# Kernel optimization log

Measured on AMD Instinct MI355X. Metric: run time of the kernel, lower is better.

The kernel has to match this reference:

```python
import jax, jax.numpy as jnp
import numpy as np

B, S, H = 2, 2048, 2048
NH, NKV, HD = 16, 8, 128        # head_dim = H // NH
WINDOW = 1024                    # sliding window size
THETA = 100000.0                 # rope_theta (RotaryEmbedding base)


def setup_inputs() -> dict:
    key = jax.random.key(0)
    ks = jax.random.split(key, 5)
    hidden = jax.random.normal(ks[0], (B, S, H), jnp.float32)
    # fused QKV projection: [H, NH*HD + 2*NKV*HD]
    W_pack = jax.random.normal(ks[1], (H, NH * HD + 2 * NKV * HD), jnp.float32) * (H ** -0.5)
    W_o = jax.random.normal(ks[2], (NH * HD, H), jnp.float32) * ((NH * HD) ** -0.5)
    # per-KV-head 2-tap causal conv weights, softmax-normalized (as in nn.Parameter init)
    conv_k = jax.nn.softmax(jax.random.normal(ks[3], (NKV, 2), jnp.float32), axis=-1)
    conv_v = jax.nn.softmax(jax.random.normal(ks[4], (NKV, 2), jnp.float32), axis=-1)
    return {"hidden": hidden, "W_pack": W_pack, "W_o": W_o, "conv_k": conv_k, "conv_v": conv_v}


def _rope(x, cos, sin):
    # x: (b, s, h, d); cos/sin: (s, d//2); non-interleaved (rotate-half) form
    d2 = x.shape[-1] // 2
    x1, x2 = x[..., :d2], x[..., d2:]
    c = cos[None, :, None, :]
    s = sin[None, :, None, :]
    return jnp.concatenate([x1 * c - x2 * s, x2 * c + x1 * s], axis=-1)


def _causal_conv2(x, w):
    # x: (b, s, kv, d); w: (kv, 2). out[t] = w0*x[t-1] + w1*x[t], zero-padded at t=0
    x_prev = jnp.pad(x, ((0, 0), (1, 0), (0, 0), (0, 0)))[:, :-1]
    return w[None, None, :, 0:1] * x_prev + w[None, None, :, 1:2] * x


def reference(hidden, W_pack, W_o, conv_k, conv_v):
    b, s, _ = hidden.shape
    qkv = hidden @ W_pack                                  # (b, s, NH*HD + 2*NKV*HD)
    q = qkv[..., : NH * HD].reshape(b, s, NH, HD)
    k = qkv[..., NH * HD : NH * HD + NKV * HD].reshape(b, s, NKV, HD)
    v = qkv[..., NH * HD + NKV * HD :].reshape(b, s, NKV, HD)

    inv_freq = 1.0 / (THETA ** (jnp.arange(0, HD, 2, dtype=jnp.float32) / HD))
    freqs = jnp.outer(jnp.arange(s, dtype=jnp.float32), inv_freq)  # (s, HD/2)
    cos, sin = jnp.cos(freqs), jnp.sin(freqs)
    q = _rope(q, cos, sin)
    k = _rope(k, cos, sin)

    # learned 2-tap causal conv mixing adjacent K/V states, per KV head
    k = _causal_conv2(k, conv_k)
    v = _causal_conv2(v, conv_v)

    # GQA: repeat kv heads to match query heads
    group = NH // NKV
    k = jnp.repeat(k, group, axis=2)  # (b, s, NH, HD)
    v = jnp.repeat(v, group, axis=2)

    scores = jnp.einsum('bqhd,bkhd->bhqk', q, k) / jnp.sqrt(jnp.float32(HD))
    i = jnp.arange(s)[:, None]
    j = jnp.arange(s)[None, :]
    mask = (j <= i) & (i - j < WINDOW)  # causal sliding-window mask
    scores = jnp.where(mask[None, None], scores, jnp.finfo(scores.dtype).min)
    probs = jax.nn.softmax(scores, axis=-1)
    out = jnp.einsum('bhqk,bkhd->bqhd', probs, v).reshape(b, s, NH * HD)
    return out @ W_o
```

## Files before the change

kernel.cpp:

```cpp
#include <hip/hip_runtime.h>

#define DI __device__ __forceinline__

typedef unsigned short u16;
typedef __attribute__((ext_vector_type(8))) short s16x8;
typedef __attribute__((ext_vector_type(8))) unsigned short u16x8;
typedef __attribute__((ext_vector_type(4))) float f32x4;
typedef __attribute__((ext_vector_type(16))) float f32x16;

DI u16 f2bf(float x) {
  union { float f; unsigned u; } a; a.f = x;
  unsigned r = a.u + 0x7FFFu + ((a.u >> 16) & 1u);
  return (u16)(r >> 16);
}
DI float bf2f(u16 u) {
  union { unsigned u; float f; } a; a.u = ((unsigned)u) << 16;
  return a.f;
}
DI void gload16(const void* g, void* l) {
  __builtin_amdgcn_global_load_lds(
      (const __attribute__((address_space(1))) unsigned int*)g,
      (__attribute__((address_space(3))) unsigned int*)l, 16, 0, 0);
}
DI f32x4 mfma16(s16x8 a, s16x8 b, f32x4 c) {
  return __builtin_amdgcn_mfma_f32_16x16x32_bf16(a, b, c, 0, 0, 0);
}
DI f32x16 mfma32(s16x8 a, s16x8 b, f32x16 c) {
  return __builtin_amdgcn_mfma_f32_32x32x16_bf16(a, b, c, 0, 0, 0);
}

DI void store_out(float* p, float v) { *p = v; }
DI void store_out(u16* p, float v) { *p = f2bf(v); }

#define SBAR() asm volatile("s_barrier" ::: "memory")
#define WAIT_LGKM0() do { asm volatile("s_waitcnt lgkmcnt(0)" ::: "memory"); \
                          __builtin_amdgcn_sched_barrier(0); } while (0)

__global__ void cvt_kernel(const float* __restrict__ in, u16* __restrict__ out, int n8) {
  int i = blockIdx.x * 256 + threadIdx.x;
  if (i >= n8) return;
  const float4* p = (const float4*)in + (size_t)i * 2;
  float4 a = p[0], b = p[1];
  u16x8 o;
  o[0] = f2bf(a.x); o[1] = f2bf(a.y); o[2] = f2bf(a.z); o[3] = f2bf(a.w);
  o[4] = f2bf(b.x); o[5] = f2bf(b.y); o[6] = f2bf(b.z); o[7] = f2bf(b.w);
  *((u16x8*)out + i) = o;
}

__global__ void cvt_t_kernel(const float* __restrict__ W, u16* __restrict__ Wt, int R, int C) {
  __shared__ u16 tile[64][65];
  int c0 = blockIdx.x * 64, r0 = blockIdx.y * 64;
  int t = threadIdx.x;
#pragma unroll
  for (int i = 0; i < 16; ++i) {
    int flat = i * 256 + t;
    int r = flat >> 6, c = flat & 63;
    tile[r][c] = f2bf(W[(size_t)(r0 + r) * C + (c0 + c)]);
  }
  __syncthreads();
#pragma unroll
  for (int i = 0; i < 16; ++i) {
    int flat = i * 256 + t;
    int c = flat >> 6, r = flat & 63;
    Wt[(size_t)(c0 + c) * R + (r0 + r)] = tile[r][c];
  }
}

__global__ void rope_table_kernel(float* __restrict__ cosT, float* __restrict__ sinT) {
  int i = blockIdx.x * 256 + threadIdx.x;
  int s = i >> 6, d = i & 63;
  float inv = expf(-(float)d * (11.5129254649702295f / 64.f));
  float f = (float)s * inv;
  cosT[i] = cosf(f);
  sinT[i] = sinf(f);
}

template <typename OutT>
__global__ __launch_bounds__(512, 2) void gemm8p_kernel(
    const u16* __restrict__ A, const u16* __restrict__ Bt, OutT* __restrict__ C,
    int M, int N, int K) {
  __shared__ __align__(16) char lds[131072];
  int nwg = gridDim.x;
  int bid = blockIdx.x;
  int cpx = nwg >> 3;
  int swz = (bid & 7) * cpx + (bid >> 3);
  int ntn = N >> 8;
  int bm = swz / ntn, bn = swz - bm * ntn;
  int m0 = bm << 8, n0 = bn << 8;
  int t = threadIdx.x, w = t >> 6, l = t & 63;
  int wm = w >> 2, wn = w & 3;
  int NT = K >> 6;

  unsigned offA[2][2], offB[2][2];
  int cA[2][2], cB[2][2];
#pragma unroll
  for (int h = 0; h < 2; ++h)
#pragma unroll
    for (int i = 0; i < 2; ++i) {
      int c = i * 16 + h * 8 + w;
      cA[h][i] = c;
      int d = c * 1024 + l * 16;
      int s = d ^ (((d >> 9) & 1) << 5);
      offA[h][i] = (unsigned)(m0 + (s >> 7)) * (unsigned)(K * 2) + (unsigned)(s & 127);
      int c2 = ((w >> 2) << 3) + (w & 3) + h * 4 + i * 16;
      cB[h][i] = c2;
      int d2 = c2 * 1024 + l * 16;
      int s2 = d2 ^ (((d2 >> 9) & 1) << 5);
      offB[h][i] = (unsigned)(n0 + (s2 >> 7)) * (unsigned)(K * 2) + (unsigned)(s2 & 127);
    }
  const char* Ab = (const char*)A;
  const char* Bb = (const char*)Bt;

#define STAGE_A(tile, h) do { int _t = (tile); if (_t < NT) {                  \
    unsigned _k = (unsigned)_t * 128u;                                          \
    char* _ba = lds + ((_t & 1) << 16);                                         \
    gload16(Ab + (size_t)(offA[h][0] + _k), _ba + cA[h][0] * 1024);             \
    gload16(Ab + (size_t)(offA[h][1] + _k), _ba + cA[h][1] * 1024); } } while (0)
#define STAGE_B(tile, h) do { int _t = (tile); if (_t < NT) {                  \
    unsigned _k = (unsigned)_t * 128u;                                          \
    char* _bb = lds + ((_t & 1) << 16) + 32768;                                 \
    gload16(Bb + (size_t)(offB[h][0] + _k), _bb + cB[h][0] * 1024);             \
    gload16(Bb + (size_t)(offB[h][1] + _k), _bb + cB[h][1] * 1024); } } while (0)

  int lanemix = (((l & 15) << 7) + ((l >> 4) << 4)) ^ ((l & 4) << 3);

  f32x4 acc[8][4] = {};
  s16x8 af[4][2], b0f[2][2], b1f[2][2];

  STAGE_A(0, 0); STAGE_B(0, 0); STAGE_A(0, 1); STAGE_B(0, 1);
  STAGE_A(1, 0); STAGE_B(1, 0); STAGE_A(1, 1);
  asm volatile("s_waitcnt vmcnt(6)" ::: "memory");
  SBAR();

  for (int tt = 0; tt < NT; ++tt) {
    const char* ldsA = lds + ((tt & 1) << 16);
    const char* ldsB = ldsA + 32768;
    const char* Ard = ldsA + (wm << 14) + lanemix;
    const char* Brd = ldsB + (wn << 13) + lanemix;

#pragma unroll
    for (int mf = 0; mf < 4; ++mf) {
      af[mf][0] = *(const s16x8*)(Ard + mf * 2048);
      af[mf][1] = *(const s16x8*)(Ard + mf * 2048 + 64);
    }
#pragma unroll
    for (int nf = 0; nf < 2; ++nf) {
      b0f[nf][0] = *(const s16x8*)(Brd + nf * 2048);
      b0f[nf][1] = *(const s16x8*)(Brd + nf * 2048 + 64);
    }
    STAGE_B(tt + 1, 1);
    SBAR();
    WAIT_LGKM0();
    __builtin_amdgcn_s_setprio(1);
#pragma unroll
    for (int mf = 0; mf < 4; ++mf)
#pragma unroll
      for (int nf = 0; nf < 2; ++nf) {
        acc[mf][nf] = mfma16(af[mf][0], b0f[nf][0], acc[mf][nf]);
        acc[mf][nf] = mfma16(af[mf][1], b0f[nf][1], acc[mf][nf]);
      }
    __builtin_amdgcn_s_setprio(0);
    SBAR();

#pragma unroll
    for (int nf = 0; nf < 2; ++nf) {
      b1f[nf][0] = *(const s16x8*)(Brd + (nf + 2) * 2048);
      b1f[nf][1] = *(const s16x8*)(Brd + (nf + 2) * 2048 + 64);
    }
    STAGE_A(tt + 2, 0);
    SBAR();
    WAIT_LGKM0();
    __builtin_amdgcn_s_setprio(1);
#pragma unroll
    for (int mf = 0; mf < 4; ++mf)
#pragma unroll
      for (int nf = 0; nf < 2; ++nf) {
        acc[mf][nf + 2] = mfma16(af[mf][0], b1f[nf][0], acc[mf][nf + 2]);
        acc[mf][nf + 2] = mfma16(af[mf][1], b1f[nf][1], acc[mf][nf + 2]);
      }
    __builtin_amdgcn_s_setprio(0);
    SBAR();

#pragma unroll
    for (int mf = 0; mf < 4; ++mf) {
      af[mf][0] = *(const s16x8*)(Ard + (mf + 4) * 2048);
      af[mf][1] = *(const s16x8*)(Ard + (mf + 4) * 2048 + 64);
    }
    STAGE_B(tt + 2, 0);
    SBAR();
    WAIT_LGKM0();
    __builtin_amdgcn_s_setprio(1);
#pragma unroll
    for (int mf = 0; mf < 4; ++mf)
#pragma unroll
      for (int nf = 0; nf < 2; ++nf) {
        acc[mf + 4][nf] = mfma16(af[mf][0], b0f[nf][0], acc[mf + 4][nf]);
        acc[mf + 4][nf] = mfma16(af[mf][1], b0f[nf][1], acc[mf + 4][nf]);
      }
    __builtin_amdgcn_s_setprio(0);
    SBAR();

    STAGE_A(tt + 2, 1);
    SBAR();
    WAIT_LGKM0();
    __builtin_amdgcn_s_setprio(1);
#pragma unroll
    for (int mf = 0; mf < 4; ++mf)
#pragma unroll
      for (int nf = 0; nf < 2; ++nf) {
        acc[mf + 4][nf + 2] = mfma16(af[mf][0], b1f[nf][0], acc[mf + 4][nf + 2]);
        acc[mf + 4][nf + 2] = mfma16(af[mf][1], b1f[nf][1], acc[mf + 4][nf + 2]);
      }
    __builtin_amdgcn_s_setprio(0);
    if (tt < NT - 2) asm volatile("s_waitcnt vmcnt(6)" ::: "memory");
    else             asm volatile("s_waitcnt vmcnt(0)" ::: "memory");
    SBAR();
  }
#undef STAGE_A
#undef STAGE_B

#pragma unroll
  for (int mf = 0; mf < 8; ++mf)
#pragma unroll
    for (int nf = 0; nf < 4; ++nf) {
      int col = n0 + wn * 64 + nf * 16 + (l & 15);
#pragma unroll
      for (int j = 0; j < 4; ++j) {
        int row = m0 + wm * 128 + mf * 16 + (l >> 4) * 4 + j;
        store_out(C + (size_t)row * N + col, acc[mf][nf][j]);
      }
    }
}

__global__ void ropeconv_kernel(const u16* __restrict__ qkv, const float* __restrict__ cosT,
                                const float* __restrict__ sinT, const float* __restrict__ convk,
                                u16* __restrict__ qb, u16* __restrict__ kb) {
  const float qs = 0.08838834764831845f;
  int row = blockIdx.x;
  int b = row >> 11, s = row & 2047;
  int t = threadIdx.x;
  const u16* qr = qkv + (size_t)row * 4096;
  u16* qo = qb + (size_t)row * 2048;
#pragma unroll
  for (int i = 0; i < 4; ++i) {
    int p = i * 256 + t;
    int h = p >> 6, d = p & 63;
    float x1 = bf2f(qr[h * 128 + d]), x2 = bf2f(qr[h * 128 + 64 + d]);
    float c = cosT[s * 64 + d], sn = sinT[s * 64 + d];
    qo[h * 128 + d] = f2bf((x1 * c - x2 * sn) * qs);
    qo[h * 128 + 64 + d] = f2bf((x2 * c + x1 * sn) * qs);
  }
  const u16* kr = qr + 2048;
#pragma unroll
  for (int i = 0; i < 2; ++i) {
    int p = i * 256 + t;
    int h = p >> 6, d = p & 63;
    float c = cosT[s * 64 + d], sn = sinT[s * 64 + d];
    float x1 = bf2f(kr[h * 128 + d]), x2 = bf2f(kr[h * 128 + 64 + d]);
    float r1 = x1 * c - x2 * sn, r2 = x2 * c + x1 * sn;
    float p1 = 0.f, p2 = 0.f;
    if (s > 0) {
      const u16* kp = kr - 4096;
      float cp = cosT[(s - 1) * 64 + d], sp = sinT[(s - 1) * 64 + d];
      float y1 = bf2f(kp[h * 128 + d]), y2 = bf2f(kp[h * 128 + 64 + d]);
      p1 = y1 * cp - y2 * sp;
      p2 = y2 * cp + y1 * sp;
    }
    float w0 = convk[h * 2], w1 = convk[h * 2 + 1];
    size_t o = (((size_t)b * 8 + h) * 2048 + s) * 128;
    kb[o + d] = f2bf(w0 * p1 + w1 * r1);
    kb[o + 64 + d] = f2bf(w0 * p2 + w1 * r2);
  }
}

__global__ void vtrans_kernel(const u16* __restrict__ qkv, const float* __restrict__ convv,
                              u16* __restrict__ vt) {
  __shared__ u16 lt[128][72];
  int st = blockIdx.x, bh = blockIdx.y;
  int b = bh >> 3, h = bh & 7;
  int s0 = st * 64;
  int t = threadIdx.x;
  float w0 = convv[h * 2], w1 = convv[h * 2 + 1];
#pragma unroll
  for (int i = 0; i < 32; ++i) {
    int flat = i * 256 + t;
    int sl = flat >> 7, d = flat & 127;
    int s = s0 + sl;
    int row = b * 2048 + s;
    float x = bf2f(qkv[(size_t)row * 4096 + 3072 + h * 128 + d]);
    float xp = (s > 0) ? bf2f(qkv[(size_t)(row - 1) * 4096 + 3072 + h * 128 + d]) : 0.f;
    lt[d][sl] = f2bf(w0 * xp + w1 * x);
  }
  __syncthreads();
#pragma unroll
  for (int i = 0; i < 32; ++i) {
    int flat = i * 256 + t;
    int d = flat >> 6, sl = flat & 63;
    vt[((size_t)(b * 8 + h) * 128 + d) * 2048 + s0 + sl] = lt[d][sl];
  }
}

__global__ __launch_bounds__(256, 2) void attn2_kernel(
    const u16* __restrict__ qb, const u16* __restrict__ kbuf, const u16* __restrict__ vt,
    u16* __restrict__ ao) {
  __shared__ __align__(16) char lds[65536];
  int qt = blockIdx.x, bh = blockIdx.y;
  int b = bh >> 4, h = bh & 15, kh = h >> 1;
  int t = threadIdx.x, w = t >> 6, l = t & 63;
  int i0 = qt * 128;
  int qbase = i0 + w * 32;
  int lq = l & 31, hi = l >> 5;
  int xorc = (l & 7) << 4;
  const char* Kg = (const char*)(kbuf + (size_t)(b * 8 + kh) * 2048 * 128);
  const char* Vg = (const char*)(vt + (size_t)(b * 8 + kh) * 128 * 2048);

  s16x8 qf[8];
  {
    const u16* qp = qb + ((size_t)(b * 2048 + qbase + lq)) * 2048 + h * 128 + 8 * hi;
#pragma unroll
    for (int kc = 0; kc < 8; ++kc) qf[kc] = *(const s16x8*)(qp + kc * 16);
  }

  unsigned ksrc[4], vsrc[4], kdst[4], vdst[4];
#pragma unroll
  for (int i = 0; i < 4; ++i) {
    int c = w * 4 + i;
    int row = c * 4 + (l >> 4);
    int colb = (l & 15) * 16;
    ksrc[i] = (unsigned)(row * 256 + (colb ^ ((row & 7) << 4)));
    kdst[i] = (unsigned)(c * 1024);
    int d = c * 8 + (l >> 3);
    int cb2 = (l & 7) * 16;
    vsrc[i] = (unsigned)(d * 4096 + (cb2 ^ ((d & 7) << 4)));
    vdst[i] = (unsigned)(16384 + c * 1024);
  }

#define STAGEKV(tile, buf) do { int _j2 = (tile) << 6;                          \
    char* _lb = lds + ((buf) << 15);                                             \
    const char* _ks = Kg + (size_t)_j2 * 256;                                    \
    const char* _vs = Vg + (size_t)_j2 * 2;                                      \
    gload16(_ks + ksrc[0], _lb + kdst[0]); gload16(_vs + vsrc[0], _lb + vdst[0]);\
    gload16(_ks + ksrc[1], _lb + kdst[1]); gload16(_vs + vsrc[1], _lb + vdst[1]);\
    gload16(_ks + ksrc[2], _lb + kdst[2]); gload16(_vs + vsrc[2], _lb + vdst[2]);\
    gload16(_ks + ksrc[3], _lb + kdst[3]); gload16(_vs + vsrc[3], _lb + vdst[3]);\
  } while (0)

  int lo = i0 - 1023; if (lo < 0) lo = 0;
  int tk0 = lo >> 6, tk1 = (i0 + 127) >> 6;

  f32x16 acco[4] = {};
  float ls0 = 0.f, ls1 = 0.f, ls2 = 0.f, ls3 = 0.f;

  int cur = 0;
  STAGEKV(tk0, 0);
  asm volatile("s_waitcnt vmcnt(0)" ::: "memory");
  SBAR();

  for (int tk = tk0; tk <= tk1; ++tk) {
    int j0 = tk << 6;
    if (tk < tk1) STAGEKV(tk + 1, cur ^ 1);
    bool relevant = (j0 <= qbase + 31) && (j0 + 63 >= qbase - 1023);
    if (relevant) {
      const char* Kl = lds + (cur << 15);
      const char* Vl = Kl + 16384;
      const char* Krow = Kl + lq * 256;
      f32x16 ps0 = {}, ps1 = {};
      __builtin_amdgcn_s_setprio(1);
#pragma unroll
      for (int kc = 0; kc < 8; ++kc) {
        s16x8 kf = *(const s16x8*)(Krow + ((kc * 32 + hi * 16) ^ xorc));
        ps0 = mfma32(kf, qf[kc], ps0);
      }
#pragma unroll
      for (int kc = 0; kc < 8; ++kc) {
        s16x8 kf = *(const s16x8*)(Krow + 8192 + ((kc * 32 + hi * 16) ^ xorc));
        ps1 = mfma32(kf, qf[kc], ps1);
      }
      __builtin_amdgcn_s_setprio(0);
      bool domask = (j0 + 63 > qbase) || (qbase + 31 - j0 >= 1024);
      int di0 = qbase + lq - j0;
      float pe[32];
#pragma unroll
      for (int r = 0; r < 16; ++r) {
        float s0 = ps0[r], s1 = ps1[r];
        if (domask) {
          int crow = (r & 3) + 8 * (r >> 2) + 4 * hi;
          if ((unsigned)(di0 - crow) >= 1024u) s0 = -1e30f;
          if ((unsigned)(di0 - 32 - crow) >= 1024u) s1 = -1e30f;
        }
        float e0 = __expf(s0), e1 = __expf(s1);
        pe[r] = e0; pe[16 + r] = e1;
        if ((r & 3) == 0) { ls0 += e0 + e1; }
        else if ((r & 3) == 1) { ls1 += e0 + e1; }
        else if ((r & 3) == 2) { ls2 += e0 + e1; }
        else { ls3 += e0 + e1; }
      }
      unsigned pk[16];
#pragma unroll
      for (int p = 0; p < 16; ++p) {
        asm("v_cvt_pk_bf16_f32 %0, %1, %2" : "=v"(pk[p]) : "v"(pe[2 * p]), "v"(pe[2 * p + 1]));
      }
      s16x8 pa[4];
#pragma unroll
      for (int ks = 0; ks < 4; ++ks) {
        int base = (ks >> 1) * 8 + (ks & 1) * 4;
        unsigned keep0 = hi ? pk[base + 2] : pk[base + 0];
        unsigned keep1 = hi ? pk[base + 3] : pk[base + 1];
        unsigned send0 = hi ? pk[base + 0] : pk[base + 2];
        unsigned send1 = hi ? pk[base + 1] : pk[base + 3];
        unsigned recv0 = (unsigned)__shfl_xor((int)send0, 32);
        unsigned recv1 = (unsigned)__shfl_xor((int)send1, 32);
        union { unsigned u[4]; s16x8 v; } pu;
        pu.u[0] = hi ? recv0 : keep0;
        pu.u[1] = hi ? recv1 : keep1;
        pu.u[2] = hi ? keep0 : recv0;
        pu.u[3] = hi ? keep1 : recv1;
        pa[ks] = pu.v;
      }
      __builtin_amdgcn_s_setprio(1);
#pragma unroll
      for (int db = 0; db < 4; ++db) {
        const char* Vrow = Vl + db * 4096 + lq * 128;
#pragma unroll
        for (int ks = 0; ks < 4; ++ks) {
          s16x8 vf = *(const s16x8*)(Vrow + ((ks * 32 + hi * 16) ^ xorc));
          acco[db] = mfma32(pa[ks], vf, acco[db]);
        }
      }
      __builtin_amdgcn_s_setprio(0);
    }
    asm volatile("s_waitcnt vmcnt(0)" ::: "memory");
    SBAR();
    cur ^= 1;
  }
#undef STAGEKV

  float lrow = (ls0 + ls1) + (ls2 + ls3);
  float lt2 = lrow + __shfl_xor(lrow, 32);
  float rinv = 1.f / lt2;
#pragma unroll
  for (int r = 0; r < 16; ++r) {
    int qidx = (r & 3) + 8 * (r >> 2) + 4 * hi;
    float rv = __shfl(rinv, qidx);
    int i = qbase + qidx;
    u16* orow = ao + ((size_t)(b * 2048 + i)) * 2048 + h * 128 + lq;
#pragma unroll
    for (int db = 0; db < 4; ++db)
      orow[db * 32] = f2bf(acco[db][r] * rv);
  }
}

extern "C" void kernel_launch(void* const* d_in, const int* in_sizes, int n_in,
                              void* d_out, int out_size, void* d_ws, size_t ws_size,
                              hipStream_t stream) {
  (void)in_sizes; (void)n_in; (void)out_size; (void)ws_size;
  const float* hidden = (const float*)d_in[0];
  const float* W_pack = (const float*)d_in[1];
  const float* W_o    = (const float*)d_in[2];
  const float* conv_k = (const float*)d_in[3];
  const float* conv_v = (const float*)d_in[4];

  char* ws = (char*)d_ws;
  const size_t MB = 1u << 20;
  u16* hA    = (u16*)(ws + 0);
  u16* wpT   = (u16*)(ws + 16 * MB);
  u16* woT   = (u16*)(ws + 32 * MB);
  u16* qkv   = (u16*)(ws + 40 * MB);
  u16* qb    = (u16*)(ws + 72 * MB);
  u16* kbuf  = (u16*)(ws + 88 * MB);
  u16* vtb   = (u16*)(ws + 96 * MB);
  float* cosT = (float*)(ws + 104 * MB);
  float* sinT = (float*)(ws + 104 * MB + 524288);
  u16* attnb = qkv;

  cvt_kernel<<<4096, 256, 0, stream>>>(hidden, hA, 1048576);
  cvt_t_kernel<<<dim3(64, 32), 256, 0, stream>>>(W_pack, wpT, 2048, 4096);
  cvt_t_kernel<<<dim3(32, 32), 256, 0, stream>>>(W_o, woT, 2048, 2048);
  rope_table_kernel<<<512, 256, 0, stream>>>(cosT, sinT);
  gemm8p_kernel<u16><<<256, 512, 0, stream>>>(hA, wpT, qkv, 4096, 4096, 2048);
  ropeconv_kernel<<<4096, 256, 0, stream>>>(qkv, cosT, sinT, conv_k, qb, kbuf);
  vtrans_kernel<<<dim3(32, 16), 256, 0, stream>>>(qkv, conv_v, vtb);
  attn2_kernel<<<dim3(16, 32), 256, 0, stream>>>(qb, kbuf, vtb, attnb);
  gemm8p_kernel<float><<<128, 512, 0, stream>>>(attnb, woT, (float*)d_out,
                                                4096, 2048, 2048);
}
```

Baseline: 229.2 us.

## Replace GEMM with 4-stage ring pipeline and merge prep kernels

Merges the input conversion, weight transposes and rope table into one prep launch, and merges the rope/conv and V-transpose kernels into one launch. The GEMM is rewritten as a 4-buffer ring with K-tiles of 32 and a single barrier per iteration instead of four. The output GEMM uses a 256x128 tile so it launches 256 workgroups instead of 128, and the epilogue writes 4 values per store instead of one. The aim is less launch overhead, fewer barriers and better occupancy in the output projection, at the cost of more loop iterations and new LDS swizzle logic that could introduce bank conflicts or bugs.

```diff
diff --git a/kernel.cpp b/kernel.cpp
--- a/kernel.cpp
+++ b/kernel.cpp
@@ -29,274 +29,219 @@
   return __builtin_amdgcn_mfma_f32_32x32x16_bf16(a, b, c, 0, 0, 0);
 }
 
-DI void store_out(float* p, float v) { *p = v; }
-DI void store_out(u16* p, float v) { *p = f2bf(v); }
+DI void store4(u16* p, f32x4 v) {
+  union { u16 u[4]; unsigned long long ll; } o;
+  o.u[0] = f2bf(v[0]); o.u[1] = f2bf(v[1]); o.u[2] = f2bf(v[2]); o.u[3] = f2bf(v[3]);
+  *(unsigned long long*)p = o.ll;
+}
+DI void store4(float* p, f32x4 v) { *(f32x4*)p = v; }
 
 #define SBAR() asm volatile("s_barrier" ::: "memory")
-#define WAIT_LGKM0() do { asm volatile("s_waitcnt lgkmcnt(0)" ::: "memory"); \
-                          __builtin_amdgcn_sched_barrier(0); } while (0)
-
-__global__ void cvt_kernel(const float* __restrict__ in, u16* __restrict__ out, int n8) {
-  int i = blockIdx.x * 256 + threadIdx.x;
-  if (i >= n8) return;
-  const float4* p = (const float4*)in + (size_t)i * 2;
-  float4 a = p[0], b = p[1];
-  u16x8 o;
-  o[0] = f2bf(a.x); o[1] = f2bf(a.y); o[2] = f2bf(a.z); o[3] = f2bf(a.w);
-  o[4] = f2bf(b.x); o[5] = f2bf(b.y); o[6] = f2bf(b.z); o[7] = f2bf(b.w);
-  *((u16x8*)out + i) = o;
-}
-
-__global__ void cvt_t_kernel(const float* __restrict__ W, u16* __restrict__ Wt, int R, int C) {
-  __shared__ u16 tile[64][65];
-  int c0 = blockIdx.x * 64, r0 = blockIdx.y * 64;
+
+__global__ __launch_bounds__(256) void prep_kernel(
+    const float* __restrict__ hidden, const float* __restrict__ W_pack,
+    const float* __restrict__ W_o, u16* __restrict__ hA, u16* __restrict__ wpT,
+    u16* __restrict__ woT, float* __restrict__ cosT, float* __restrict__ sinT) {
+  int bi = blockIdx.x;
   int t = threadIdx.x;
-#pragma unroll
-  for (int i = 0; i < 16; ++i) {
-    int flat = i * 256 + t;
-    int r = flat >> 6, c = flat & 63;
-    tile[r][c] = f2bf(W[(size_t)(r0 + r) * C + (c0 + c)]);
-  }
-  __syncthreads();
-#pragma unroll
-  for (int i = 0; i < 16; ++i) {
-    int flat = i * 256 + t;
-    int c = flat >> 6, r = flat & 63;
-    Wt[(size_t)(c0 + c) * R + (r0 + r)] = tile[r][c];
-  }
-}
-
-__global__ void rope_table_kernel(float* __restrict__ cosT, float* __restrict__ sinT) {
-  int i = blockIdx.x * 256 + threadIdx.x;
-  int s = i >> 6, d = i & 63;
-  float inv = expf(-(float)d * (11.5129254649702295f / 64.f));
-  float f = (float)s * inv;
-  cosT[i] = cosf(f);
-  sinT[i] = sinf(f);
-}
-
-template <typename OutT>
-__global__ __launch_bounds__(512, 2) void gemm8p_kernel(
+  if (bi < 4096) {
+    int i = bi * 256 + t;
+    const float4* p = (const float4*)hidden + (size_t)i * 2;
+    float4 a = p[0], b = p[1];
+    u16x8 o;
+    o[0] = f2bf(a.x); o[1] = f2bf(a.y); o[2] = f2bf(a.z); o[3] = f2bf(a.w);
+    o[4] = f2bf(b.x); o[5] = f2bf(b.y); o[6] = f2bf(b.z); o[7] = f2bf(b.w);
+    *((u16x8*)hA + i) = o;
+  } else if (bi < 7168) {
+    const float* W; u16* Wt; int R, C, c0, r0;
+    if (bi < 6144) {
+      int idx = bi - 4096;
+      W = W_pack; Wt = wpT; R = 2048; C = 4096;
+      c0 = (idx & 63) * 64; r0 = (idx >> 6) * 64;
+    } else {
+      int idx = bi - 6144;
+      W = W_o; Wt = woT; R = 2048; C = 2048;
+      c0 = (idx & 31) * 64; r0 = (idx >> 5) * 64;
+    }
+    __shared__ u16 tile[64][65];
+#pragma unroll
+    for (int i = 0; i < 16; ++i) {
+      int flat = i * 256 + t;
+      int r = flat >> 6, c = flat & 63;
+      tile[r][c] = f2bf(W[(size_t)(r0 + r) * C + (c0 + c)]);
+    }
+    __syncthreads();
+#pragma unroll
+    for (int i = 0; i < 16; ++i) {
+      int flat = i * 256 + t;
+      int c = flat >> 6, r = flat & 63;
+      Wt[(size_t)(c0 + c) * R + (r0 + r)] = tile[r][c];
+    }
+  } else {
+    int i = (bi - 7168) * 256 + t;
+    int s = i >> 6, d = i & 63;
+    float inv = expf(-(float)d * (11.5129254649702295f / 64.f));
+    float f = (float)s * inv;
+    cosT[i] = cosf(f);
+    sinT[i] = sinf(f);
+  }
+}
+
+template <int BN, typename OutT>
+__global__ __launch_bounds__(512, 2) void gemm_ring_kernel(
     const u16* __restrict__ A, const u16* __restrict__ Bt, OutT* __restrict__ C,
     int M, int N, int K) {
-  __shared__ __align__(16) char lds[131072];
-  int nwg = gridDim.x;
-  int bid = blockIdx.x;
+  constexpr int BSZ = 16384 + BN * 64;
+  constexpr int NB = BN / 64;
+  constexpr int BU = BN / 128;
+  __shared__ __align__(16) char lds[4 * BSZ];
+  int nwg = gridDim.x, bid = blockIdx.x;
   int cpx = nwg >> 3;
   int swz = (bid & 7) * cpx + (bid >> 3);
-  int ntn = N >> 8;
+  int ntn = N / BN;
   int bm = swz / ntn, bn = swz - bm * ntn;
-  int m0 = bm << 8, n0 = bn << 8;
+  int m0 = bm << 8, n0 = bn * BN;
   int t = threadIdx.x, w = t >> 6, l = t & 63;
   int wm = w >> 2, wn = w & 3;
-  int NT = K >> 6;
-
-  unsigned offA[2][2], offB[2][2];
-  int cA[2][2], cB[2][2];
-#pragma unroll
-  for (int h = 0; h < 2; ++h)
-#pragma unroll
-    for (int i = 0; i < 2; ++i) {
-      int c = i * 16 + h * 8 + w;
-      cA[h][i] = c;
-      int d = c * 1024 + l * 16;
-      int s = d ^ (((d >> 9) & 1) << 5);
-      offA[h][i] = (unsigned)(m0 + (s >> 7)) * (unsigned)(K * 2) + (unsigned)(s & 127);
-      int c2 = ((w >> 2) << 3) + (w & 3) + h * 4 + i * 16;
-      cB[h][i] = c2;
-      int d2 = c2 * 1024 + l * 16;
-      int s2 = d2 ^ (((d2 >> 9) & 1) << 5);
-      offB[h][i] = (unsigned)(n0 + (s2 >> 7)) * (unsigned)(K * 2) + (unsigned)(s2 & 127);
-    }
+  int NT = K >> 5;
+
+  unsigned srcA[2], srcB[BU];
+  unsigned scol = (unsigned)(((t & 3) ^ ((t >> 3) & 3)) << 4);
+#pragma unroll
+  for (int u = 0; u < 2; ++u)
+    srcA[u] = (unsigned)(m0 + u * 128 + (t >> 2)) * (unsigned)(K * 2) + scol;
+#pragma unroll
+  for (int u = 0; u < BU; ++u)
+    srcB[u] = (unsigned)(n0 + u * 128 + (t >> 2)) * (unsigned)(K * 2) + scol;
+  unsigned dstT = (unsigned)(t * 16);
   const char* Ab = (const char*)A;
   const char* Bb = (const char*)Bt;
 
-#define STAGE_A(tile, h) do { int _t = (tile); if (_t < NT) {                  \
-    unsigned _k = (unsigned)_t * 128u;                                          \
-    char* _ba = lds + ((_t & 1) << 16);                                         \
-    gload16(Ab + (size_t)(offA[h][0] + _k), _ba + cA[h][0] * 1024);             \
-    gload16(Ab + (size_t)(offA[h][1] + _k), _ba + cA[h][1] * 1024); } } while (0)
-#define STAGE_B(tile, h) do { int _t = (tile); if (_t < NT) {                  \
-    unsigned _k = (unsigned)_t * 128u;                                          \
-    char* _bb = lds + ((_t & 1) << 16) + 32768;                                 \
-    gload16(Bb + (size_t)(offB[h][0] + _k), _bb + cB[h][0] * 1024);             \
-    gload16(Bb + (size_t)(offB[h][1] + _k), _bb + cB[h][1] * 1024); } } while (0)
-
-  int lanemix = (((l & 15) << 7) + ((l >> 4) << 4)) ^ ((l & 4) << 3);
-
-  f32x4 acc[8][4] = {};
-  s16x8 af[4][2], b0f[2][2], b1f[2][2];
-
-  STAGE_A(0, 0); STAGE_B(0, 0); STAGE_A(0, 1); STAGE_B(0, 1);
-  STAGE_A(1, 0); STAGE_B(1, 0); STAGE_A(1, 1);
-  asm volatile("s_waitcnt vmcnt(6)" ::: "memory");
+#define STAGE(tile) do { int _t = (tile); if (_t < NT) {                        \
+    char* _bb = lds + (size_t)(_t & 3) * BSZ;                                    \
+    unsigned _k = (unsigned)_t * 64u;                                            \
+    gload16(Ab + (size_t)(srcA[0] + _k), _bb + dstT);                            \
+    gload16(Ab + (size_t)(srcA[1] + _k), _bb + 8192 + dstT);                     \
+    gload16(Bb + (size_t)(srcB[0] + _k), _bb + 16384 + dstT);                    \
+    if (BU > 1) gload16(Bb + (size_t)(srcB[BU - 1] + _k), _bb + 24576 + dstT);   \
+  } } while (0)
+
+  int lanemix = ((l & 15) << 6) + ((((l >> 4) ^ ((l >> 1) & 3))) << 4);
+
+  f32x4 acc[8][NB] = {};
+  s16x8 af[8], bfr[NB];
+
+  STAGE(0); STAGE(1); STAGE(2);
+  if (BN == 256) asm volatile("s_waitcnt vmcnt(8)" ::: "memory");
+  else           asm volatile("s_waitcnt vmcnt(6)" ::: "memory");
   SBAR();
 
   for (int tt = 0; tt < NT; ++tt) {
-    const char* ldsA = lds + ((tt & 1) << 16);
-    const char* ldsB = ldsA + 32768;
-    const char* Ard = ldsA + (wm << 14) + lanemix;
-    const char* Brd = ldsB + (wn << 13) + lanemix;
-
-#pragma unroll
-    for (int mf = 0; mf < 4; ++mf) {
-      af[mf][0] = *(const s16x8*)(Ard + mf * 2048);
-      af[mf][1] = *(const s16x8*)(Ard + mf * 2048 + 64);
-    }
-#pragma unroll
-    for (int nf = 0; nf < 2; ++nf) {
-      b0f[nf][0] = *(const s16x8*)(Brd + nf * 2048);
-      b0f[nf][1] = *(const s16x8*)(Brd + nf * 2048 + 64);
-    }
-    STAGE_B(tt + 1, 1);
-    SBAR();
-    WAIT_LGKM0();
+    char* buf = lds + (size_t)(tt & 3) * BSZ;
+    const char* Ard = buf + wm * 8192 + lanemix;
+    const char* Brd = buf + 16384 + wn * (BN / 4) * 64 + lanemix;
+    STAGE(tt + 3);
+#pragma unroll
+    for (int mf = 0; mf < 8; ++mf) af[mf] = *(const s16x8*)(Ard + mf * 1024);
+#pragma unroll
+    for (int nf = 0; nf < NB; ++nf) bfr[nf] = *(const s16x8*)(Brd + nf * 1024);
     __builtin_amdgcn_s_setprio(1);
 #pragma unroll
-    for (int mf = 0; mf < 4; ++mf)
-#pragma unroll
-      for (int nf = 0; nf < 2; ++nf) {
-        acc[mf][nf] = mfma16(af[mf][0], b0f[nf][0], acc[mf][nf]);
-        acc[mf][nf] = mfma16(af[mf][1], b0f[nf][1], acc[mf][nf]);
-      }
+    for (int mf = 0; mf < 8; ++mf)
+#pragma unroll
+      for (int nf = 0; nf < NB; ++nf)
+        acc[mf][nf] = mfma16(bfr[nf], af[mf], acc[mf][nf]);
     __builtin_amdgcn_s_setprio(0);
-    SBAR();
-
-#pragma unroll
-    for (int nf = 0; nf < 2; ++nf) {
-      b1f[nf][0] = *(const s16x8*)(Brd + (nf + 2) * 2048);
-      b1f[nf][1] = *(const s16x8*)(Brd + (nf + 2) * 2048 + 64);
-    }
-    STAGE_A(tt + 2, 0);
-    SBAR();
-    WAIT_LGKM0();
-    __builtin_amdgcn_s_setprio(1);
-#pragma unroll
-    for (int mf = 0; mf < 4; ++mf)
-#pragma unroll
-      for (int nf = 0; nf < 2; ++nf) {
-        acc[mf][nf + 2] = mfma16(af[mf][0], b1f[nf][0], acc[mf][nf + 2]);
-        acc[mf][nf + 2] = mfma16(af[mf][1], b1f[nf][1], acc[mf][nf + 2]);
-      }
-    __builtin_amdgcn_s_setprio(0);
-    SBAR();
-
-#pragma unroll
-    for (int mf = 0; mf < 4; ++mf) {
-      af[mf][0] = *(const s16x8*)(Ard + (mf + 4) * 2048);
-      af[mf][1] = *(const s16x8*)(Ard + (mf + 4) * 2048 + 64);
-    }
-    STAGE_B(tt + 2, 0);
-    SBAR();
-    WAIT_LGKM0();
-    __builtin_amdgcn_s_setprio(1);
-#pragma unroll
-    for (int mf = 0; mf < 4; ++mf)
-#pragma unroll
-      for (int nf = 0; nf < 2; ++nf) {
-        acc[mf + 4][nf] = mfma16(af[mf][0], b0f[nf][0], acc[mf + 4][nf]);
-        acc[mf + 4][nf] = mfma16(af[mf][1], b0f[nf][1], acc[mf + 4][nf]);
-      }
-    __builtin_amdgcn_s_setprio(0);
-    SBAR();
-
-    STAGE_A(tt + 2, 1);
-    SBAR();
-    WAIT_LGKM0();
-    __builtin_amdgcn_s_setprio(1);
-#pragma unroll
-    for (int mf = 0; mf < 4; ++mf)
-#pragma unroll
-      for (int nf = 0; nf < 2; ++nf) {
-        acc[mf + 4][nf + 2] = mfma16(af[mf][0], b1f[nf][0], acc[mf + 4][nf + 2]);
-        acc[mf + 4][nf + 2] = mfma16(af[mf][1], b1f[nf][1], acc[mf + 4][nf + 2]);
-      }
-    __builtin_amdgcn_s_setprio(0);
-    if (tt < NT - 2) asm volatile("s_waitcnt vmcnt(6)" ::: "memory");
-    else             asm volatile("s_waitcnt vmcnt(0)" ::: "memory");
-    SBAR();
-  }
-#undef STAGE_A
-#undef STAGE_B
-
-#pragma unroll
-  for (int mf = 0; mf < 8; ++mf)
-#pragma unroll
-    for (int nf = 0; nf < 4; ++nf) {
-      int col = n0 + wn * 64 + nf * 16 + (l & 15);
-#pragma unroll
-      for (int j = 0; j < 4; ++j) {
-        int row = m0 + wm * 128 + mf * 16 + (l >> 4) * 4 + j;
-        store_out(C + (size_t)row * N + col, acc[mf][nf][j]);
-      }
-    }
-}
-
-__global__ void ropeconv_kernel(const u16* __restrict__ qkv, const float* __restrict__ cosT,
-                                const float* __restrict__ sinT, const float* __restrict__ convk,
-                                u16* __restrict__ qb, u16* __restrict__ kb) {
-  const float qs = 0.08838834764831845f;
-  int row = blockIdx.x;
-  int b = row >> 11, s = row & 2047;
+    if (tt + 1 < NT) {
+      if (tt + 3 < NT) {
+        if (BN == 256) asm volatile("s_waitcnt vmcnt(8)" ::: "memory");
+        else           asm volatile("s_waitcnt vmcnt(6)" ::: "memory");
+      } else if (tt + 2 < NT) {
+        if (BN == 256) asm volatile("s_waitcnt vmcnt(4)" ::: "memory");
+        else           asm volatile("s_waitcnt vmcnt(3)" ::: "memory");
+      } else {
+        asm volatile("s_waitcnt vmcnt(0)" ::: "memory");
+      }
+      SBAR();
+    }
+  }
+#undef STAGE
+
+#pragma unroll
+  for (int mf = 0; mf < 8; ++mf) {
+    int row = m0 + wm * 128 + mf * 16 + (l & 15);
+    OutT* crow = C + (size_t)row * N + n0 + wn * (BN / 4) + (l >> 4) * 4;
+#pragma unroll
+    for (int nf = 0; nf < NB; ++nf) store4(crow + nf * 16, acc[mf][nf]);
+  }
+}
+
+__global__ void rcvt_kernel(const u16* __restrict__ qkv, const float* __restrict__ cosT,
+                            const float* __restrict__ sinT, const float* __restrict__ convk,
+                            const float* __restrict__ convv,
+                            u16* __restrict__ qb, u16* __restrict__ kb,
+                            u16* __restrict__ vt) {
   int t = threadIdx.x;
-  const u16* qr = qkv + (size_t)row * 4096;
-  u16* qo = qb + (size_t)row * 2048;
-#pragma unroll
-  for (int i = 0; i < 4; ++i) {
-    int p = i * 256 + t;
-    int h = p >> 6, d = p & 63;
-    float x1 = bf2f(qr[h * 128 + d]), x2 = bf2f(qr[h * 128 + 64 + d]);
-    float c = cosT[s * 64 + d], sn = sinT[s * 64 + d];
-    qo[h * 128 + d] = f2bf((x1 * c - x2 * sn) * qs);
-    qo[h * 128 + 64 + d] = f2bf((x2 * c + x1 * sn) * qs);
-  }
-  const u16* kr = qr + 2048;
-#pragma unroll
-  for (int i = 0; i < 2; ++i) {
-    int p = i * 256 + t;
-    int h = p >> 6, d = p & 63;
-    float c = cosT[s * 64 + d], sn = sinT[s * 64 + d];
-    float x1 = bf2f(kr[h * 128 + d]), x2 = bf2f(kr[h * 128 + 64 + d]);
-    float r1 = x1 * c - x2 * sn, r2 = x2 * c + x1 * sn;
-    float p1 = 0.f, p2 = 0.f;
-    if (s > 0) {
-      const u16* kp = kr - 4096;
-      float cp = cosT[(s - 1) * 64 + d], sp = sinT[(s - 1) * 64 + d];
-      float y1 = bf2f(kp[h * 128 + d]), y2 = bf2f(kp[h * 128 + 64 + d]);
-      p1 = y1 * cp - y2 * sp;
-      p2 = y2 * cp + y1 * sp;
-    }
-    float w0 = convk[h * 2], w1 = convk[h * 2 + 1];
-    size_t o = (((size_t)b * 8 + h) * 2048 + s) * 128;
-    kb[o + d] = f2bf(w0 * p1 + w1 * r1);
-    kb[o + 64 + d] = f2bf(w0 * p2 + w1 * r2);
-  }
-}
-
-__global__ void vtrans_kernel(const u16* __restrict__ qkv, const float* __restrict__ convv,
-                              u16* __restrict__ vt) {
-  __shared__ u16 lt[128][72];
-  int st = blockIdx.x, bh = blockIdx.y;
-  int b = bh >> 3, h = bh & 7;
-  int s0 = st * 64;
-  int t = threadIdx.x;
-  float w0 = convv[h * 2], w1 = convv[h * 2 + 1];
-#pragma unroll
-  for (int i = 0; i < 32; ++i) {
-    int flat = i * 256 + t;
-    int sl = flat >> 7, d = flat & 127;
-    int s = s0 + sl;
-    int row = b * 2048 + s;
-    float x = bf2f(qkv[(size_t)row * 4096 + 3072 + h * 128 + d]);
-    float xp = (s > 0) ? bf2f(qkv[(size_t)(row - 1) * 4096 + 3072 + h * 128 + d]) : 0.f;
-    lt[d][sl] = f2bf(w0 * xp + w1 * x);
-  }
-  __syncthreads();
-#pragma unroll
-  for (int i = 0; i < 32; ++i) {
-    int flat = i * 256 + t;
-    int d = flat >> 6, sl = flat & 63;
-    vt[((size_t)(b * 8 + h) * 128 + d) * 2048 + s0 + sl] = lt[d][sl];
+  if (blockIdx.x < 4096) {
+    const float qs = 0.08838834764831845f;
+    int row = blockIdx.x;
+    int b = row >> 11, s = row & 2047;
+    const u16* qr = qkv + (size_t)row * 4096;
+    u16* qo = qb + (size_t)row * 2048;
+#pragma unroll
+    for (int i = 0; i < 4; ++i) {
+      int p = i * 256 + t;
+      int h = p >> 6, d = p & 63;
+      float x1 = bf2f(qr[h * 128 + d]), x2 = bf2f(qr[h * 128 + 64 + d]);
+      float c = cosT[s * 64 + d], sn = sinT[s * 64 + d];
+      qo[h * 128 + d] = f2bf((x1 * c - x2 * sn) * qs);
+      qo[h * 128 + 64 + d] = f2bf((x2 * c + x1 * sn) * qs);
+    }
+    const u16* kr = qr + 2048;
+#pragma unroll
+    for (int i = 0; i < 2; ++i) {
+      int p = i * 256 + t;
+      int h = p >> 6, d = p & 63;
+      float c = cosT[s * 64 + d], sn = sinT[s * 64 + d];
+      float x1 = bf2f(kr[h * 128 + d]), x2 = bf2f(kr[h * 128 + 64 + d]);
+      float r1 = x1 * c - x2 * sn, r2 = x2 * c + x1 * sn;
+      float p1 = 0.f, p2 = 0.f;
+      if (s > 0) {
+        const u16* kp = kr - 4096;
+        float cp = cosT[(s - 1) * 64 + d], sp = sinT[(s - 1) * 64 + d];
+        float y1 = bf2f(kp[h * 128 + d]), y2 = bf2f(kp[h * 128 + 64 + d]);
+        p1 = y1 * cp - y2 * sp;
+        p2 = y2 * cp + y1 * sp;
+      }
+      float w0 = convk[h * 2], w1 = convk[h * 2 + 1];
+      size_t o = (((size_t)b * 8 + h) * 2048 + s) * 128;
+      kb[o + d] = f2bf(w0 * p1 + w1 * r1);
+      kb[o + 64 + d] = f2bf(w0 * p2 + w1 * r2);
+    }
+  } else {
+    __shared__ u16 lt[128][72];
+    int idx = blockIdx.x - 4096;
+    int st = idx & 31, bh = idx >> 5;
+    int b = bh >> 3, h = bh & 7;
+    int s0 = st * 64;
+    float w0 = convv[h * 2], w1 = convv[h * 2 + 1];
+#pragma unroll
+    for (int i = 0; i < 32; ++i) {
+      int flat = i * 256 + t;
+      int sl = flat >> 7, d = flat & 127;
+      int s = s0 + sl;
+      int row = b * 2048 + s;
+      float x = bf2f(qkv[(size_t)row * 4096 + 3072 + h * 128 + d]);
+      float xp = (s > 0) ? bf2f(qkv[(size_t)(row - 1) * 4096 + 3072 + h * 128 + d]) : 0.f;
+      lt[d][sl] = f2bf(w0 * xp + w1 * x);
+    }
+    __syncthreads();
+#pragma unroll
+    for (int i = 0; i < 32; ++i) {
+      int flat = i * 256 + t;
+      int d = flat >> 6, sl = flat & 63;
+      vt[((size_t)(b * 8 + h) * 128 + d) * 2048 + s0 + sl] = lt[d][sl];
+    }
   }
 }
 
@@ -473,14 +418,10 @@
   float* sinT = (float*)(ws + 104 * MB + 524288);
   u16* attnb = qkv;
 
-  cvt_kernel<<<4096, 256, 0, stream>>>(hidden, hA, 1048576);
-  cvt_t_kernel<<<dim3(64, 32), 256, 0, stream>>>(W_pack, wpT, 2048, 4096);
-  cvt_t_kernel<<<dim3(32, 32), 256, 0, stream>>>(W_o, woT, 2048, 2048);
-  rope_table_kernel<<<512, 256, 0, stream>>>(cosT, sinT);
-  gemm8p_kernel<u16><<<256, 512, 0, stream>>>(hA, wpT, qkv, 4096, 4096, 2048);
-  ropeconv_kernel<<<4096, 256, 0, stream>>>(qkv, cosT, sinT, conv_k, qb, kbuf);
-  vtrans_kernel<<<dim3(32, 16), 256, 0, stream>>>(qkv, conv_v, vtb);
+  prep_kernel<<<7680, 256, 0, stream>>>(hidden, W_pack, W_o, hA, wpT, woT, cosT, sinT);
+  gemm_ring_kernel<256, u16><<<256, 512, 0, stream>>>(hA, wpT, qkv, 4096, 4096, 2048);
+  rcvt_kernel<<<4608, 256, 0, stream>>>(qkv, cosT, sinT, conv_k, conv_v, qb, kbuf, vtb);
   attn2_kernel<<<dim3(16, 32), 256, 0, stream>>>(qb, kbuf, vtb, attnb);
-  gemm8p_kernel<float><<<128, 512, 0, stream>>>(attnb, woT, (float*)d_out,
-                                                4096, 2048, 2048);
-}
+  gemm_ring_kernel<128, float><<<256, 512, 0, stream>>>(attnb, woT, (float*)d_out,
+                                                        4096, 2048, 2048);
+}
```

After: 192.4 us. -16.0%, faster.
